# Performance work log

Hardware: AMD Instinct MI355X
Metric: run time of the kernel (lower is better)

Reference implementation:

```python
import jax, jax.numpy as jnp
import numpy as np

C1 = 0.01 ** 2
C2 = 0.03 ** 2
IN_CH = 3
WIN = 11
LEVELS = 5


def _gauss_kernel(k=WIN, sigma=1.5, c=IN_CH):
    ax = np.arange(k, dtype=np.float32) - (k - 1) / 2.0
    g = np.exp(-(ax ** 2) / (2.0 * sigma ** 2))
    g = g / g.sum()
    w2d = np.outer(g, g).astype(np.float32)  # [k,k]
    return jnp.asarray(np.tile(w2d[None, None], (c, 1, 1, 1)))  # [C,1,k,k]


def _dwconv(x, w):
    # depthwise (grouped) conv, 'same' padding for odd kernel
    pad = (w.shape[-1] - 1) // 2
    return jax.lax.conv_general_dilated(
        x, w, window_strides=(1, 1), padding=[(pad, pad), (pad, pad)],
        feature_group_count=x.shape[1],
        dimension_numbers=("NCHW", "OIHW", "NCHW"))


def _ssim_loss(i1, i2, w):
    m1 = _dwconv(i1, w)
    m2 = _dwconv(i2, w)
    m1sq = m1 * m1
    m2sq = m2 * m2
    m12 = m1 * m2
    s1 = _dwconv(i1 * i1, w) - m1sq
    s2 = _dwconv(i2 * i2, w) - m2sq
    s12 = _dwconv(i1 * i2, w) - m12
    ssim = (2 * m12 + C1) * (2 * s12 + C2) / ((m1sq + m2sq + C1) * (s1 + s2 + C2))
    return 1.0 - ssim.mean()


def _avg_pool2(x):
    B, C, H, W = x.shape
    return x.reshape(B, C, H // 2, 2, W // 2, 2).mean(axis=(3, 5))


def setup_inputs() -> dict:
    key = jax.random.key(0)
    k1, k2 = jax.random.split(key)
    img1 = jax.random.uniform(k1, (16, IN_CH, 512, 512), dtype=jnp.float32)
    img2 = jax.random.uniform(k2, (16, IN_CH, 512, 512), dtype=jnp.float32)
    inp = {"img1": img1, "img2": img2}
    for i in range(LEVELS):
        inp[f"g{i}"] = _gauss_kernel()
    return inp


def reference(img1, img2, g0, g1, g2, g3, g4):
    loss = jnp.asarray(0.0, dtype=img1.dtype)
    for w in (g0, g1, g2, g3, g4):
        loss = loss + _ssim_loss(img1, img2, w)
        img1 = _avg_pool2(img1)
        img2 = _avg_pool2(img2)
    return loss
```

## Files before the change

kernel.cpp:

```cpp
#include <hip/hip_runtime.h>
#include <math.h>

#define WIN 11
#define PAD 5
#define TW 64

typedef float v2f __attribute__((ext_vector_type(2)));

struct GW { float g[WIN]; };

template<bool EMIT, int TH>
__device__ __forceinline__ float ssim_wave_tile(
    const float* __restrict__ p1, const float* __restrict__ p2,
    int W, int X0, int Y0, const GW& gw, float4* __restrict__ rb,
    float* __restrict__ o1a, float* __restrict__ o1b, int Wout)
{
    const int lane = threadIdx.x & 63;
    const int gx = X0 + lane;
    const bool cval = gx < W;
    const int hx   = (lane < 5) ? (X0 - 5 + lane) : (X0 + 59 + lane);
    const bool hval = (lane < 10) && ((unsigned)hx < (unsigned)W);
    const int hpos = (lane < 5) ? lane : (64 + lane);
    const int cpos = 5 + lane;

    float vMp[11], vSp[11], vMq[11], vSq[11];
#pragma unroll
    for (int k = 0; k < 11; ++k) { vMp[k] = 0.f; vSp[k] = 0.f; vMq[k] = 0.f; vSq[k] = 0.f; }

    float part = 0.f;
    float pprev = 0.f, qprev = 0.f;

    auto LOAD = [&](int t, float& oa, float& ob, float& oah, float& obh) {
        int y = Y0 - PAD + t;
        oa = 0.f; ob = 0.f; oah = 0.f; obh = 0.f;
        if ((unsigned)y < (unsigned)W) {
            const float* r1 = p1 + (size_t)y * W;
            const float* r2 = p2 + (size_t)y * W;
            if (cval) { oa  = r1[gx]; ob  = r2[gx]; }
            if (hval) { oah = r1[hx]; obh = r2[hx]; }
        }
    };

    float a0, b0, ah0, bh0;
    float a1, b1, ah1, bh1;
    LOAD(0, a0, b0, ah0, bh0);
    LOAD(1, a1, b1, ah1, bh1);

#pragma unroll 2
    for (int t = 0; t < TH + 10; ++t) {
        float a2, b2, ah2, bh2;
        LOAD(t + 2, a2, b2, ah2, bh2);

        float p = a0 + b0, q = a0 - b0;
        rb[cpos] = make_float4(p, q, p * p, q * q);
        if (lane < 10) {
            float ph = ah0 + bh0, qh = ah0 - bh0;
            rb[hpos] = make_float4(ph, qh, ph * ph, qh * qh);
        }
        __builtin_amdgcn_wave_barrier();

        v2f hM = {0.f, 0.f}, hS = {0.f, 0.f};
#pragma unroll
        for (int j = 0; j < WIN; ++j) {
            float4 v = rb[lane + j];
            v2f vm = { v.x, v.y };
            v2f vs = { v.z, v.w };
            v2f g2 = { gw.g[j], gw.g[j] };
            hM = __builtin_elementwise_fma(g2, vm, hM);
            hS = __builtin_elementwise_fma(g2, vs, hS);
        }
        __builtin_amdgcn_wave_barrier();
        float hp = hM.x, hq = hM.y, hpp = hS.x, hqq = hS.y;

#pragma unroll
        for (int k = 0; k < 11; ++k) {
            float g = gw.g[10 - k];
            vMp[k] = fmaf(g, hp,  vMp[k]);
            vSp[k] = fmaf(g, hpp, vSp[k]);
            vMq[k] = fmaf(g, hq,  vMq[k]);
            vSq[k] = fmaf(g, hqq, vSq[k]);
        }

        if (EMIT) {
            if (t >= 6 && t <= TH + 4 && (t & 1) == 0) {
                float sp_ = p + pprev, sq_ = q + qprev;
                float sp2 = sp_ + __shfl_down(sp_, 1, 64);
                float sq2 = sq_ + __shfl_down(sq_, 1, 64);
                if ((lane & 1) == 0) {
                    float P = sp2 * 0.25f, Q = sq2 * 0.25f;
                    int yo = (t - 6) >> 1;
                    size_t oo = (size_t)((Y0 >> 1) + yo) * Wout + ((X0 >> 1) + (lane >> 1));
                    o1a[oo] = (P + Q) * 0.5f;
                    o1b[oo] = (P - Q) * 0.5f;
                }
            }
            pprev = p; qprev = q;
        }

        if (t >= 10) {
            int o = t - 10;
            bool yok = (unsigned)(Y0 + o) < (unsigned)W;
            float Mp = vMp[0], Sp_ = vSp[0], Mq = vMq[0], Sq_ = vSq[0];
            const float C1v = 1e-4f, C2v = 9e-4f;
            float A = Mp * Mp, B = Mq * Mq;
            float ABp = A + B, ABm = A - B;
            float SSp = Sp_ + Sq_, SSm = Sp_ - Sq_;
            float n1 = fmaf(0.5f, ABm, C1v);
            float n2 = fmaf(0.5f, SSm - ABm, C2v);
            float e1 = fmaf(0.5f, ABp, C1v);
            float e2 = fmaf(0.5f, SSp - ABp, C2v);
            float v = (n1 * n2) * __builtin_amdgcn_rcpf(e1 * e2);
            part += (cval && yok) ? v : 0.f;
        }

#pragma unroll
        for (int k = 0; k < 10; ++k) {
            vMp[k] = vMp[k + 1]; vSp[k] = vSp[k + 1];
            vMq[k] = vMq[k + 1]; vSq[k] = vSq[k + 1];
        }
        vMp[10] = 0.f; vSp[10] = 0.f; vMq[10] = 0.f; vSq[10] = 0.f;

        a0 = a1; b0 = b1; ah0 = ah1; bh0 = bh1;
        a1 = a2; b1 = b2; ah1 = ah2; bh1 = bh2;
    }

    return part;
}

__global__ __launch_bounds__(256, 4) void ssim_l0_kernel(
    const float* __restrict__ i1, const float* __restrict__ i2,
    float* __restrict__ a1, float* __restrict__ b1,
    double* __restrict__ acc, GW gw)
{
    __shared__ float4 rbs[4][80];
    const int wid = threadIdx.x >> 6;
    const int w = blockIdx.x * 4 + wid;
    const int img = w >> 7;
    const int tt = w & 127;
    const int tx = tt & 7, ty = tt >> 3;
    const size_t off  = (size_t)img * 512 * 512;
    const size_t ooff = (size_t)img * 256 * 256;

    float part = ssim_wave_tile<true, 32>(i1 + off, i2 + off, 512, tx * 64, ty * 32,
                                          gw, rbs[wid], a1 + ooff, b1 + ooff, 256);
#pragma unroll
    for (int o = 32; o > 0; o >>= 1) part += __shfl_down(part, o, 64);
    if ((threadIdx.x & 63) == 0) atomicAdd(acc, (double)part);
}

__global__ __launch_bounds__(256, 4) void ssim_rest_kernel(
    const float* __restrict__ a1, const float* __restrict__ b1,
    const float* __restrict__ a2, const float* __restrict__ b2,
    const float* __restrict__ a3, const float* __restrict__ b3,
    const float* __restrict__ a4, const float* __restrict__ b4,
    double* __restrict__ acc, GW gw)
{
    __shared__ float4 rbs[4][80];
    const int wid = threadIdx.x >> 6;
    const int w = blockIdx.x * 4 + wid;
    const int img = w / 86;
    const int r = w - img * 86;
    int lvl, tx, ty;
    if (r < 64)      { lvl = 1; tx = r & 3;  ty = r >> 2; }
    else if (r < 80) { lvl = 2; int s = r - 64; tx = s & 1; ty = s >> 1; }
    else if (r < 84) { lvl = 3; tx = 0; ty = r - 80; }
    else             { lvl = 4; tx = 0; ty = r - 84; }
    const int W = 512 >> lvl;
    const float* p1; const float* p2;
    switch (lvl) {
      case 1:  p1 = a1; p2 = b1; break;
      case 2:  p1 = a2; p2 = b2; break;
      case 3:  p1 = a3; p2 = b3; break;
      default: p1 = a4; p2 = b4; break;
    }
    const size_t off = (size_t)img * W * W;

    float part = ssim_wave_tile<false, 16>(p1 + off, p2 + off, W, tx * 64, ty * 16,
                                           gw, rbs[wid], nullptr, nullptr, 0);
#pragma unroll
    for (int o = 32; o > 0; o >>= 1) part += __shfl_down(part, o, 64);
    if ((threadIdx.x & 63) == 0) atomicAdd(acc + lvl, (double)part);
}

__global__ __launch_bounds__(256) void pool_rest_kernel(
    const float* __restrict__ a1, const float* __restrict__ b1,
    float* __restrict__ a2, float* __restrict__ b2,
    float* __restrict__ a3, float* __restrict__ b3,
    float* __restrict__ a4, float* __restrict__ b4)
{
    __shared__ float l2[32][33];
    __shared__ float l3[16][17];
    const int tid = threadIdx.x;
    const int im = blockIdx.y;
    const int tb = blockIdx.x;
    const int tx = tb & 3, ty = tb >> 2;
    const bool second = im >= 48;
    const int ii = second ? im - 48 : im;
    const float* src = (second ? b1 : a1) + (size_t)ii * 256 * 256;
    float* o2 = (second ? b2 : a2) + (size_t)ii * 128 * 128;
    float* o3 = (second ? b3 : a3) + (size_t)ii * 64 * 64;
    float* o4 = (second ? b4 : a4) + (size_t)ii * 32 * 32;
    const int X0 = tx * 64, Y0 = ty * 64;

#pragma unroll
    for (int k = 0; k < 2; ++k) {
        int idx = tid + k * 256;
        int xp = idx & 15;
        int yo = idx >> 4;
        const float* rp = src + (size_t)(Y0 + 2 * yo) * 256 + (X0 + 4 * xp);
        float4 r0 = *(const float4*)rp;
        float4 r1 = *(const float4*)(rp + 256);
        float v0 = (r0.x + r0.y + r1.x + r1.y) * 0.25f;
        float v1 = (r0.z + r0.w + r1.z + r1.w) * 0.25f;
        l2[yo][2 * xp]     = v0;
        l2[yo][2 * xp + 1] = v1;
        float2* op = (float2*)(o2 + (size_t)((Y0 >> 1) + yo) * 128 + ((X0 >> 1) + 2 * xp));
        *op = make_float2(v0, v1);
    }
    __syncthreads();
    {
        int xo = tid & 15, yo = tid >> 4;
        if (yo < 16) {
            float v = (l2[2*yo][2*xo] + l2[2*yo][2*xo+1] +
                       l2[2*yo+1][2*xo] + l2[2*yo+1][2*xo+1]) * 0.25f;
            l3[yo][xo] = v;
            o3[(size_t)((Y0 >> 2) + yo) * 64 + ((X0 >> 2) + xo)] = v;
        }
    }
    __syncthreads();
    if (tid < 64) {
        int xo = tid & 7, yo = tid >> 3;
        float v = (l3[2*yo][2*xo] + l3[2*yo][2*xo+1] +
                   l3[2*yo+1][2*xo] + l3[2*yo+1][2*xo+1]) * 0.25f;
        o4[(size_t)((Y0 >> 3) + yo) * 32 + ((X0 >> 3) + xo)] = v;
    }
}

__global__ void final_kernel(const double* __restrict__ acc, float* __restrict__ out)
{
    double loss = 0.0;
#pragma unroll
    for (int l = 0; l < 5; ++l) {
        double cnt = 48.0 * (double)(512 >> l) * (double)(512 >> l);
        loss += 1.0 - acc[l] / cnt;
    }
    out[0] = (float)loss;
}

extern "C" void kernel_launch(void* const* d_in, const int* in_sizes, int n_in,
                              void* d_out, int out_size, void* d_ws, size_t ws_size,
                              hipStream_t stream)
{
    const float* img1 = (const float*)d_in[0];
    const float* img2 = (const float*)d_in[1];
    float* out = (float*)d_out;

    GW gw;
    double gs[WIN], sum = 0.0;
    for (int i = 0; i < WIN; ++i) {
        double ax = (double)i - 5.0;
        gs[i] = exp(-(ax * ax) / 4.5);
        sum += gs[i];
    }
    for (int i = 0; i < WIN; ++i) gw.g[i] = (float)(gs[i] / sum);

    double* acc = (double*)d_ws;
    float* base = (float*)((char*)d_ws + 64);
    const size_t n1 = 48ull * 256 * 256;
    const size_t n2 = 48ull * 128 * 128;
    const size_t n3 = 48ull * 64 * 64;
    const size_t n4 = 48ull * 32 * 32;
    float* a1 = base;      float* b1 = a1 + n1;
    float* a2 = b1 + n1;   float* b2 = a2 + n2;
    float* a3 = b2 + n2;   float* b3 = a3 + n3;
    float* a4 = b3 + n3;   float* b4 = a4 + n4;

    hipMemsetAsync(acc, 0, 5 * sizeof(double), stream);

    hipLaunchKernelGGL(ssim_l0_kernel, dim3(1536), dim3(256), 0, stream,
                       img1, img2, a1, b1, acc, gw);

    hipLaunchKernelGGL(pool_rest_kernel, dim3(16, 96), dim3(256), 0, stream,
                       a1, b1, a2, b2, a3, b3, a4, b4);

    hipLaunchKernelGGL(ssim_rest_kernel, dim3(264 * 4 / 4 == 264 ? 1032 : 1032), dim3(256), 0, stream,
                       a1, b1, a2, b2, a3, b3, a4, b4, acc, gw);

    hipLaunchKernelGGL(final_kernel, dim3(1), dim3(1), 0, stream, acc, out);
}
```

Before: 298.8 us.

## Use rotating register ring for vertical accumulators and shrink LDS row buffer

Replaces the per-row shift of the 44 vertical accumulator registers with a modulo-11 rotating index, fully unrolled over 11-row blocks, so the register moves are gone. The LDS row buffer now stores only (p,q) as float2 and squares them after loading, halving LDS traffic at the cost of extra multiplies. The rest-level tiles grow from 16 to 32 rows, halving the wave count and the vertical halo overhead for levels 1-4, at the cost of less parallelism. Sched barriers are added per step, and the larger unrolled body may raise register pressure or code size.

```diff
diff --git a/kernel.cpp b/kernel.cpp
--- a/kernel.cpp
+++ b/kernel.cpp
@@ -9,12 +9,13 @@
 
 struct GW { float g[WIN]; };
 
-template<bool EMIT, int TH>
+template<bool EMIT>
 __device__ __forceinline__ float ssim_wave_tile(
     const float* __restrict__ p1, const float* __restrict__ p2,
-    int W, int X0, int Y0, const GW& gw, float4* __restrict__ rb,
+    int W, int X0, int Y0, const GW& gw, float2* __restrict__ rb,
     float* __restrict__ o1a, float* __restrict__ o1b, int Wout)
 {
+    const int TH = 32;
     const int lane = threadIdx.x & 63;
     const int gx = X0 + lane;
     const bool cval = gx < W;
@@ -46,82 +47,85 @@
     LOAD(0, a0, b0, ah0, bh0);
     LOAD(1, a1, b1, ah1, bh1);
 
-#pragma unroll 2
-    for (int t = 0; t < TH + 10; ++t) {
-        float a2, b2, ah2, bh2;
-        LOAD(t + 2, a2, b2, ah2, bh2);
-
-        float p = a0 + b0, q = a0 - b0;
-        rb[cpos] = make_float4(p, q, p * p, q * q);
-        if (lane < 10) {
-            float ph = ah0 + bh0, qh = ah0 - bh0;
-            rb[hpos] = make_float4(ph, qh, ph * ph, qh * qh);
+#pragma unroll 1
+    for (int blk = 0; blk < 4; ++blk) {
+#pragma unroll
+        for (int u = 0; u < 11; ++u) {
+            const int t = blk * 11 + u;
+
+            float a2, b2, ah2, bh2;
+            LOAD(t + 2, a2, b2, ah2, bh2);
+
+            float p = a0 + b0, q = a0 - b0;
+            rb[cpos] = make_float2(p, q);
+            if (lane < 10) {
+                float ph = ah0 + bh0, qh = ah0 - bh0;
+                rb[hpos] = make_float2(ph, qh);
+            }
+            __builtin_amdgcn_wave_barrier();
+
+            v2f hM = {0.f, 0.f}, hS = {0.f, 0.f};
+#pragma unroll
+            for (int j = 0; j < WIN; ++j) {
+                float2 v = rb[lane + j];
+                v2f vm = { v.x, v.y };
+                v2f g2 = { gw.g[j], gw.g[j] };
+                hM = __builtin_elementwise_fma(g2, vm, hM);
+                hS = __builtin_elementwise_fma(g2, vm * vm, hS);
+            }
+            __builtin_amdgcn_wave_barrier();
+            float hp = hM.x, hq = hM.y, hpp = hS.x, hqq = hS.y;
+
+#pragma unroll
+            for (int s = 0; s < 11; ++s) {
+                const int widx = 10 - ((s - u + 11) % 11);
+                float g = gw.g[widx];
+                vMp[s] = fmaf(g, hp,  vMp[s]);
+                vSp[s] = fmaf(g, hpp, vSp[s]);
+                vMq[s] = fmaf(g, hq,  vMq[s]);
+                vSq[s] = fmaf(g, hqq, vSq[s]);
+            }
+
+            if (EMIT) {
+                if (t >= 6 && t <= TH + 4 && (t & 1) == 0) {
+                    float sp_ = p + pprev, sq_ = q + qprev;
+                    float sp2 = sp_ + __shfl_down(sp_, 1, 64);
+                    float sq2 = sq_ + __shfl_down(sq_, 1, 64);
+                    if ((lane & 1) == 0) {
+                        float P = sp2 * 0.25f, Q = sq2 * 0.25f;
+                        int yo = (t - 6) >> 1;
+                        size_t oo = (size_t)((Y0 >> 1) + yo) * Wout + ((X0 >> 1) + (lane >> 1));
+                        o1a[oo] = (P + Q) * 0.5f;
+                        o1b[oo] = (P - Q) * 0.5f;
+                    }
+                }
+                pprev = p; qprev = q;
+            }
+
+            {
+                int o = t - 10;
+                if ((unsigned)o < (unsigned)TH) {
+                    bool yok = (unsigned)(Y0 + o) < (unsigned)W;
+                    float Mp = vMp[u], Sp_ = vSp[u], Mq = vMq[u], Sq_ = vSq[u];
+                    const float C1v = 1e-4f, C2v = 9e-4f;
+                    float A = Mp * Mp, B = Mq * Mq;
+                    float ABp = A + B, ABm = A - B;
+                    float SSp = Sp_ + Sq_, SSm = Sp_ - Sq_;
+                    float n1 = fmaf(0.5f, ABm, C1v);
+                    float n2 = fmaf(0.5f, SSm - ABm, C2v);
+                    float e1 = fmaf(0.5f, ABp, C1v);
+                    float e2 = fmaf(0.5f, SSp - ABp, C2v);
+                    float v = (n1 * n2) * __builtin_amdgcn_rcpf(e1 * e2);
+                    part += (cval && yok) ? v : 0.f;
+                }
+                vMp[u] = 0.f; vSp[u] = 0.f; vMq[u] = 0.f; vSq[u] = 0.f;
+            }
+
+            a0 = a1; b0 = b1; ah0 = ah1; bh0 = bh1;
+            a1 = a2; b1 = b2; ah1 = ah2; bh1 = bh2;
+
+            __builtin_amdgcn_sched_barrier(0);
         }
-        __builtin_amdgcn_wave_barrier();
-
-        v2f hM = {0.f, 0.f}, hS = {0.f, 0.f};
-#pragma unroll
-        for (int j = 0; j < WIN; ++j) {
-            float4 v = rb[lane + j];
-            v2f vm = { v.x, v.y };
-            v2f vs = { v.z, v.w };
-            v2f g2 = { gw.g[j], gw.g[j] };
-            hM = __builtin_elementwise_fma(g2, vm, hM);
-            hS = __builtin_elementwise_fma(g2, vs, hS);
-        }
-        __builtin_amdgcn_wave_barrier();
-        float hp = hM.x, hq = hM.y, hpp = hS.x, hqq = hS.y;
-
-#pragma unroll
-        for (int k = 0; k < 11; ++k) {
-            float g = gw.g[10 - k];
-            vMp[k] = fmaf(g, hp,  vMp[k]);
-            vSp[k] = fmaf(g, hpp, vSp[k]);
-            vMq[k] = fmaf(g, hq,  vMq[k]);
-            vSq[k] = fmaf(g, hqq, vSq[k]);
-        }
-
-        if (EMIT) {
-            if (t >= 6 && t <= TH + 4 && (t & 1) == 0) {
-                float sp_ = p + pprev, sq_ = q + qprev;
-                float sp2 = sp_ + __shfl_down(sp_, 1, 64);
-                float sq2 = sq_ + __shfl_down(sq_, 1, 64);
-                if ((lane & 1) == 0) {
-                    float P = sp2 * 0.25f, Q = sq2 * 0.25f;
-                    int yo = (t - 6) >> 1;
-                    size_t oo = (size_t)((Y0 >> 1) + yo) * Wout + ((X0 >> 1) + (lane >> 1));
-                    o1a[oo] = (P + Q) * 0.5f;
-                    o1b[oo] = (P - Q) * 0.5f;
-                }
-            }
-            pprev = p; qprev = q;
-        }
-
-        if (t >= 10) {
-            int o = t - 10;
-            bool yok = (unsigned)(Y0 + o) < (unsigned)W;
-            float Mp = vMp[0], Sp_ = vSp[0], Mq = vMq[0], Sq_ = vSq[0];
-            const float C1v = 1e-4f, C2v = 9e-4f;
-            float A = Mp * Mp, B = Mq * Mq;
-            float ABp = A + B, ABm = A - B;
-            float SSp = Sp_ + Sq_, SSm = Sp_ - Sq_;
-            float n1 = fmaf(0.5f, ABm, C1v);
-            float n2 = fmaf(0.5f, SSm - ABm, C2v);
-            float e1 = fmaf(0.5f, ABp, C1v);
-            float e2 = fmaf(0.5f, SSp - ABp, C2v);
-            float v = (n1 * n2) * __builtin_amdgcn_rcpf(e1 * e2);
-            part += (cval && yok) ? v : 0.f;
-        }
-
-#pragma unroll
-        for (int k = 0; k < 10; ++k) {
-            vMp[k] = vMp[k + 1]; vSp[k] = vSp[k + 1];
-            vMq[k] = vMq[k + 1]; vSq[k] = vSq[k + 1];
-        }
-        vMp[10] = 0.f; vSp[10] = 0.f; vMq[10] = 0.f; vSq[10] = 0.f;
-
-        a0 = a1; b0 = b1; ah0 = ah1; bh0 = bh1;
-        a1 = a2; b1 = b2; ah1 = ah2; bh1 = bh2;
     }
 
     return part;
@@ -132,7 +136,7 @@
     float* __restrict__ a1, float* __restrict__ b1,
     double* __restrict__ acc, GW gw)
 {
-    __shared__ float4 rbs[4][80];
+    __shared__ float2 rbs[4][80];
     const int wid = threadIdx.x >> 6;
     const int w = blockIdx.x * 4 + wid;
     const int img = w >> 7;
@@ -141,8 +145,8 @@
     const size_t off  = (size_t)img * 512 * 512;
     const size_t ooff = (size_t)img * 256 * 256;
 
-    float part = ssim_wave_tile<true, 32>(i1 + off, i2 + off, 512, tx * 64, ty * 32,
-                                          gw, rbs[wid], a1 + ooff, b1 + ooff, 256);
+    float part = ssim_wave_tile<true>(i1 + off, i2 + off, 512, tx * 64, ty * 32,
+                                      gw, rbs[wid], a1 + ooff, b1 + ooff, 256);
 #pragma unroll
     for (int o = 32; o > 0; o >>= 1) part += __shfl_down(part, o, 64);
     if ((threadIdx.x & 63) == 0) atomicAdd(acc, (double)part);
@@ -155,16 +159,16 @@
     const float* __restrict__ a4, const float* __restrict__ b4,
     double* __restrict__ acc, GW gw)
 {
-    __shared__ float4 rbs[4][80];
+    __shared__ float2 rbs[4][80];
     const int wid = threadIdx.x >> 6;
     const int w = blockIdx.x * 4 + wid;
-    const int img = w / 86;
-    const int r = w - img * 86;
+    const int img = w / 43;
+    const int r = w - img * 43;
     int lvl, tx, ty;
-    if (r < 64)      { lvl = 1; tx = r & 3;  ty = r >> 2; }
-    else if (r < 80) { lvl = 2; int s = r - 64; tx = s & 1; ty = s >> 1; }
-    else if (r < 84) { lvl = 3; tx = 0; ty = r - 80; }
-    else             { lvl = 4; tx = 0; ty = r - 84; }
+    if (r < 32)      { lvl = 1; tx = r & 3;  ty = r >> 2; }
+    else if (r < 40) { lvl = 2; int s = r - 32; tx = s & 1; ty = s >> 1; }
+    else if (r < 42) { lvl = 3; tx = 0; ty = r - 40; }
+    else             { lvl = 4; tx = 0; ty = 0; }
     const int W = 512 >> lvl;
     const float* p1; const float* p2;
     switch (lvl) {
@@ -175,8 +179,8 @@
     }
     const size_t off = (size_t)img * W * W;
 
-    float part = ssim_wave_tile<false, 16>(p1 + off, p2 + off, W, tx * 64, ty * 16,
-                                           gw, rbs[wid], nullptr, nullptr, 0);
+    float part = ssim_wave_tile<false>(p1 + off, p2 + off, W, tx * 64, ty * 32,
+                                       gw, rbs[wid], nullptr, nullptr, 0);
 #pragma unroll
     for (int o = 32; o > 0; o >>= 1) part += __shfl_down(part, o, 64);
     if ((threadIdx.x & 63) == 0) atomicAdd(acc + lvl, (double)part);
@@ -283,7 +287,7 @@
     hipLaunchKernelGGL(pool_rest_kernel, dim3(16, 96), dim3(256), 0, stream,
                        a1, b1, a2, b2, a3, b3, a4, b4);
 
-    hipLaunchKernelGGL(ssim_rest_kernel, dim3(264 * 4 / 4 == 264 ? 1032 : 1032), dim3(256), 0, stream,
+    hipLaunchKernelGGL(ssim_rest_kernel, dim3(516), dim3(256), 0, stream,
                        a1, b1, a2, b2, a3, b3, a4, b4, acc, gw);
 
     hipLaunchKernelGGL(final_kernel, dim3(1), dim3(1), 0, stream, acc, out);
```

New measurement: 277.9 us. 1.08x faster.
